# Kernel optimization log

Hardware: AMD Instinct MI355X
Metric: run time of the kernel (lower is better)

Reference implementation:

```python
import jax, jax.numpy as jnp
import numpy as np

HEADS = 8
DIM_HEAD = 64
EPS = 1e-5

def setup_inputs() -> dict:
    key = jax.random.key(0)
    ks = jax.random.split(key, 5)
    c, inner = 320, HEADS * DIM_HEAD
    s = 0.02
    return {
        "hidden_states": jax.random.normal(ks[0], (4, c, 16, 32, 32), jnp.float32),
        "ln_w": jnp.ones((c,), jnp.float32),
        "ln_b": jnp.zeros((c,), jnp.float32),
        "Wq": jax.random.normal(ks[1], (inner, c), jnp.float32) * s,
        "Wk": jax.random.normal(ks[2], (inner, c), jnp.float32) * s,
        "Wv": jax.random.normal(ks[3], (inner, c), jnp.float32) * s,
        "Wo": jax.random.normal(ks[4], (c, inner), jnp.float32) * s,
        "bo": jnp.zeros((c,), jnp.float32),
    }

def reference(hidden_states, ln_w, ln_b, Wq, Wk, Wv, Wo, bo):
    b, c, t, h, w = hidden_states.shape
    scale = DIM_HEAD ** (-0.5)
    # (b h w) t c
    x0 = jnp.transpose(hidden_states, (0, 3, 4, 2, 1)).reshape(b * h * w, t, c)
    # LayerNorm over channel dim
    mu = jnp.mean(x0, axis=-1, keepdims=True)
    var = jnp.var(x0, axis=-1, keepdims=True)
    xn = (x0 - mu) / jnp.sqrt(var + EPS) * ln_w + ln_b
    # QKV projections (self-attention: encoder_hidden_states = normed hidden)
    q = xn @ Wq.T  # [B, t, inner]
    k = xn @ Wk.T
    v = xn @ Wv.T
    B = b * h * w
    q = q.reshape(B, t, HEADS, DIM_HEAD)
    k = k.reshape(B, t, HEADS, DIM_HEAD)
    v = v.reshape(B, t, HEADS, DIM_HEAD)
    scores = jnp.einsum("bqhd,bkhd->bhqk", q, k) * scale
    probs = jax.nn.softmax(scores, axis=-1)
    out = jnp.einsum("bhqk,bkhd->bqhd", probs, v).reshape(B, t, HEADS * DIM_HEAD)
    out = out @ Wo.T + bo
    out = out + x0  # residual (dropout p=0)
    # back to b c t h w
    return jnp.transpose(out.reshape(b, h, w, t, c), (0, 4, 3, 1, 2))
```

## Files before the change

kernel.cpp:

```cpp
#include <hip/hip_runtime.h>

#define TT 16
#define CC 320
#define NHEADS 8
#define DH 64
#define INNER 512

typedef float f32x4 __attribute__((ext_vector_type(4)));
typedef float f32x16 __attribute__((ext_vector_type(16)));
typedef short bf16x8 __attribute__((ext_vector_type(8)));
typedef unsigned short u16;

#define Z16 {0.f,0.f,0.f,0.f,0.f,0.f,0.f,0.f,0.f,0.f,0.f,0.f,0.f,0.f,0.f,0.f}

__device__ __forceinline__ float bf2f(u16 u){
    union { unsigned int i; float f; } v; v.i = ((unsigned int)u) << 16; return v.f;
}
__device__ __forceinline__ u16 f2bf(float f){
    union { float f; unsigned int i; } v; v.f = f;
    unsigned int x = v.i;
    return (u16)((x + 0x7fffu + ((x >> 16) & 1u)) >> 16);
}

__global__ __launch_bounds__(256) void k_wqkv32(const float* __restrict__ wq, const float* __restrict__ wk,
                                                const float* __restrict__ wv, u16* __restrict__ dst){
    int gid  = blockIdx.x * 256 + threadIdx.x;
    int lane = gid & 63;
    int f    = gid >> 6;
    int local = f % 12;
    int kl   = local & 1;
    int nblk = local >> 1;
    int c    = (f / 12) % 10;
    int hd   = f / 120;
    int kk   = c * 2 + kl;
    const float* W = (nblk < 2) ? wq : (nblk < 4) ? wk : wv;
    int n  = hd * DH + (nblk & 1) * 32 + (lane & 31);
    int k0 = kk * 16 + (lane >> 5) * 8;
    const float* src = W + (size_t)n * CC + k0;
    f32x4 v0 = *(const f32x4*)src;
    f32x4 v1 = *(const f32x4*)(src + 4);
    bf16x8 o;
    o[0] = (short)f2bf(v0[0]); o[1] = (short)f2bf(v0[1]);
    o[2] = (short)f2bf(v0[2]); o[3] = (short)f2bf(v0[3]);
    o[4] = (short)f2bf(v1[0]); o[5] = (short)f2bf(v1[1]);
    o[6] = (short)f2bf(v1[2]); o[7] = (short)f2bf(v1[3]);
    *(bf16x8*)(dst + (size_t)gid * 8) = o;
}

__global__ __launch_bounds__(256) void k_wo16(const float* __restrict__ wo, u16* __restrict__ dst){
    int idx  = blockIdx.x * 256 + threadIdx.x;
    int lane = idx & 63;
    int blk  = idx >> 6;
    int KT = INNER / 32;
    int n  = (blk / KT) * 16 + (lane & 15);
    int k0 = (blk % KT) * 32 + (lane >> 4) * 8;
    const float* src = wo + (size_t)n * INNER + k0;
    f32x4 v0 = *(const f32x4*)src;
    f32x4 v1 = *(const f32x4*)(src + 4);
    bf16x8 o;
    o[0] = (short)f2bf(v0[0]); o[1] = (short)f2bf(v0[1]);
    o[2] = (short)f2bf(v0[2]); o[3] = (short)f2bf(v0[3]);
    o[4] = (short)f2bf(v1[0]); o[5] = (short)f2bf(v1[1]);
    o[6] = (short)f2bf(v1[2]); o[7] = (short)f2bf(v1[3]);
    *(bf16x8*)(dst + (size_t)idx * 8) = o;
}

__global__ __launch_bounds__(256) void k_ln(const float* __restrict__ x, const float* __restrict__ lnw,
                                            const float* __restrict__ lnb, u16* __restrict__ xnf){
    __shared__ float tile[CC][37];
    __shared__ float psum[32][36];
    __shared__ float psq[32][36];
    __shared__ float meanb[32];
    __shared__ float rstdb[32];

    int wg = blockIdx.x;
    int t = wg & 15, h = (wg >> 4) & 31, b = wg >> 9;
    int tid = threadIdx.x;
    const size_t base = ((size_t)(b * CC) * TT + t) * 1024 + h * 32;

    int w4 = (tid & 7) * 4, cg = tid >> 3;
    f32x4 s4 = {0.f,0.f,0.f,0.f}, q4 = {0.f,0.f,0.f,0.f};
    for (int i = 0; i < 10; ++i){
        int c = cg * 10 + i;
        f32x4 v = *(const f32x4*)(x + base + (size_t)c * 16384 + w4);
        tile[c][w4 + 0] = v[0]; tile[c][w4 + 1] = v[1];
        tile[c][w4 + 2] = v[2]; tile[c][w4 + 3] = v[3];
        s4 += v; q4 += v * v;
    }
    psum[cg][w4 + 0] = s4[0]; psum[cg][w4 + 1] = s4[1]; psum[cg][w4 + 2] = s4[2]; psum[cg][w4 + 3] = s4[3];
    psq [cg][w4 + 0] = q4[0]; psq [cg][w4 + 1] = q4[1]; psq [cg][w4 + 2] = q4[2]; psq [cg][w4 + 3] = q4[3];
    __syncthreads();

    if (tid < 32){
        float s = 0.f, q = 0.f;
        for (int g = 0; g < 32; ++g){ s += psum[g][tid]; q += psq[g][tid]; }
        float mean = s * (1.f / CC);
        float var  = q * (1.f / CC) - mean * mean;
        meanb[tid] = mean;
        rstdb[tid] = rsqrtf(var + 1e-5f);
    }
    __syncthreads();

    int cl = tid & 63, wq_ = tid >> 6;
    float lw[5], lb[5];
    #pragma unroll
    for (int ci = 0; ci < 5; ++ci){ lw[ci] = lnw[ci * 64 + cl]; lb[ci] = lnb[ci * 64 + cl]; }
    int s_base = (b * 32 + h) * 32;
    for (int wi = 0; wi < 8; ++wi){
        int w = wq_ * 8 + wi;
        float mean = meanb[w], rstd = rstdb[w];
        int s = s_base + w;
        int row = ((s & 1) << 4) | t;
        size_t m32 = (size_t)(s >> 1);
        #pragma unroll
        for (int ci = 0; ci < 5; ++ci){
            int c = ci * 64 + cl;
            float nv = (tile[c][w] - mean) * rstd * lw[ci] + lb[ci];
            int lane = ((((c & 15) >> 3)) << 5) | row;
            xnf[((m32 * 20 + (c >> 4)) * 64 + lane) * 8 + (c & 7)] = f2bf(nv);
        }
    }
}

#define QH(w,s,r,c) smem[((((w)*2+(s))*16+(r))*72) + (c)]
#define KH(w,s,r,c) smem[9216 + ((((w)*2+(s))*16+(r))*72) + (c)]
#define VT(w,s,d,k) smem[18432 + ((((w)*2+(s))*64+(d))*36) + (k)]

__global__ __attribute__((amdgpu_flat_work_group_size(256, 256), amdgpu_waves_per_eu(2, 2)))
void k_attn(const u16* __restrict__ xnf,
            const u16* __restrict__ wqkv,
            u16* __restrict__ aof){
    __shared__ u16 smem[36864];

    const int tid  = threadIdx.x;
    const int lane = tid & 63;
    const int wid  = tid >> 6;
    const int l31  = lane & 31;
    const int h32  = lane >> 5;
    const int l15  = lane & 15;
    const int g4   = lane >> 4;
    const int m32  = blockIdx.x * 4 + wid;
    const f32x4 zero4 = {0.f, 0.f, 0.f, 0.f};

    #pragma unroll
    for (int j = 0; j < 32; ++j){
        int idx = j * 64 + lane;
        int smp = idx >> 10;
        int d   = (idx >> 4) & 63;
        VT(wid, smp, d, 16 + (idx & 15)) = 0;
    }

    bf16x8 a_f[20];
    {
        const u16* xp = xnf + ((size_t)m32 * 20 * 64 + lane) * 8;
        #pragma unroll
        for (int kk = 0; kk < 20; ++kk)
            a_f[kk] = *(const bf16x8*)(xp + kk * 512);
    }

    #define STAGE(hd_, c_) do {                                                        \
        const u16* gsrc_ = wqkv + ((size_t)((hd_) * 10 + (c_)) * 6144);                \
        u16* ldst_ = (u16*)smem + ((c_) & 1) * 6144;                                   \
        _Pragma("unroll")                                                              \
        for (int i_ = 0; i_ < 3; ++i_)                                                 \
            __builtin_amdgcn_global_load_lds(                                          \
                (const __attribute__((address_space(1))) void*)(gsrc_ + (tid + i_ * 256) * 8), \
                (__attribute__((address_space(3))) void*)(ldst_ + (tid + i_ * 256) * 8),       \
                16, 0, 0);                                                             \
    } while (0)

    for (int hd = 0; hd < NHEADS; ++hd){
        __builtin_amdgcn_sched_barrier(0);
        __builtin_amdgcn_s_barrier();
        __builtin_amdgcn_sched_barrier(0);

        STAGE(hd, 0);

        f32x16 acc[6];
        #pragma unroll
        for (int nb = 0; nb < 6; ++nb) acc[nb] = (f32x16)Z16;

        #pragma unroll
        for (int c = 0; c < 10; ++c){
            asm volatile("s_waitcnt vmcnt(0)" ::: "memory");
            __builtin_amdgcn_sched_barrier(0);
            __builtin_amdgcn_s_barrier();
            __builtin_amdgcn_sched_barrier(0);
            if (c < 9) STAGE(hd, c + 1);
            const u16* wb = (const u16*)smem + (c & 1) * 6144;
            #pragma unroll
            for (int kl = 0; kl < 2; ++kl){
                #pragma unroll
                for (int nb = 0; nb < 6; ++nb){
                    bf16x8 b = *(const bf16x8*)(wb + (nb * 2 + kl) * 512 + lane * 8);
                    acc[nb] = __builtin_amdgcn_mfma_f32_32x32x16_bf16(a_f[c * 2 + kl], b, acc[nb], 0, 0, 0);
                }
            }
            __builtin_amdgcn_sched_barrier(0);
            __builtin_amdgcn_s_barrier();
            __builtin_amdgcn_sched_barrier(0);
        }

        #pragma unroll
        for (int r = 0; r < 16; ++r){
            int row = (r & 3) + 8 * (r >> 2) + 4 * h32;
            int smp = row >> 4, tr = row & 15;
            QH(wid, smp, tr, l31)      = f2bf(acc[0][r] * 0.125f);
            QH(wid, smp, tr, 32 + l31) = f2bf(acc[1][r] * 0.125f);
            KH(wid, smp, tr, l31)      = f2bf(acc[2][r]);
            KH(wid, smp, tr, 32 + l31) = f2bf(acc[3][r]);
            VT(wid, smp, l31, tr)      = f2bf(acc[4][r]);
            VT(wid, smp, 32 + l31, tr) = f2bf(acc[5][r]);
        }

        #pragma unroll
        for (int smp = 0; smp < 2; ++smp){
            f32x4 sc = zero4;
            #pragma unroll
            for (int k0 = 0; k0 < DH; k0 += 32){
                bf16x8 qa = *(const bf16x8*)&QH(wid, smp, l15, k0 + g4 * 8);
                bf16x8 kb = *(const bf16x8*)&KH(wid, smp, l15, k0 + g4 * 8);
                sc = __builtin_amdgcn_mfma_f32_16x16x32_bf16(qa, kb, sc, 0, 0, 0);
            }
            f32x4 pr;
            #pragma unroll
            for (int r = 0; r < 4; ++r){
                float m = sc[r];
                m = fmaxf(m, __shfl_xor(m, 1)); m = fmaxf(m, __shfl_xor(m, 2));
                m = fmaxf(m, __shfl_xor(m, 4)); m = fmaxf(m, __shfl_xor(m, 8));
                float e = __expf(sc[r] - m);
                float ss = e;
                ss += __shfl_xor(ss, 1); ss += __shfl_xor(ss, 2);
                ss += __shfl_xor(ss, 4); ss += __shfl_xor(ss, 8);
                pr[r] = e / ss;
            }
            #pragma unroll
            for (int r = 0; r < 4; ++r){
                QH(wid, smp, g4 * 4 + r, l15) = f2bf(pr[r]);
                QH(wid, smp, g4 * 4 + r, 16 + l15) = 0;
            }
            bf16x8 pa = *(const bf16x8*)&QH(wid, smp, l15, g4 * 8);
            #pragma unroll
            for (int nb = 0; nb < 4; ++nb){
                bf16x8 vb = *(const bf16x8*)&VT(wid, smp, nb * 16 + l15, g4 * 8);
                f32x4 at = __builtin_amdgcn_mfma_f32_16x16x32_bf16(pa, vb, zero4, 0, 0, 0);
                #pragma unroll
                for (int r = 0; r < 4; ++r)
                    KH(wid, smp, g4 * 4 + r, nb * 16 + l15) = f2bf(at[r]);
            }
            const size_t sg = (size_t)m32 * 2 + smp;
            #pragma unroll
            for (int kkl = 0; kkl < 2; ++kkl){
                bf16x8 o8 = *(const bf16x8*)&KH(wid, smp, l15, kkl * 32 + g4 * 8);
                *(bf16x8*)(aof + ((sg * 16 + hd * 2 + kkl) * 64 + lane) * 8) = o8;
            }
        }
    }
    #undef STAGE
}

__global__ __launch_bounds__(512, 4) void k_oproj(const u16* __restrict__ aof, const u16* __restrict__ wof,
                                                  const float* __restrict__ bo, u16* __restrict__ proj){
    const int tid  = threadIdx.x;
    const int lane = tid & 63;
    const int wid  = tid >> 6;
    const int l15  = lane & 15;
    const int g4   = lane >> 4;
    const int mh   = wid >> 1;
    const int nh   = wid & 1;
    const size_t mt0 = (size_t)blockIdx.x * 8 + mh * 2;
    const size_t m0  = mt0 * 16;

    f32x4 acc[10][2];
    #pragma unroll
    for (int j = 0; j < 10; ++j){
        acc[j][0] = (f32x4){0.f,0.f,0.f,0.f};
        acc[j][1] = (f32x4){0.f,0.f,0.f,0.f};
    }

    const u16* ap = aof + (mt0 * 16 * 64 + lane) * 8;
    const u16* wp = wof + (((size_t)nh * 10 * 16) * 64 + lane) * 8;

    #pragma unroll 2
    for (int kk = 0; kk < 16; ++kk){
        bf16x8 a0 = *(const bf16x8*)(ap + kk * 512);
        bf16x8 a1 = *(const bf16x8*)(ap + (16 + kk) * 512);
        #pragma unroll
        for (int j = 0; j < 10; ++j){
            bf16x8 b = *(const bf16x8*)(wp + (j * 16 + kk) * 512);
            acc[j][0] = __builtin_amdgcn_mfma_f32_16x16x32_bf16(a0, b, acc[j][0], 0, 0, 0);
            acc[j][1] = __builtin_amdgcn_mfma_f32_16x16x32_bf16(a1, b, acc[j][1], 0, 0, 0);
        }
    }

    #pragma unroll
    for (int j = 0; j < 10; ++j){
        int c = nh * 160 + j * 16 + l15;
        float bias = bo[c];
        #pragma unroll
        for (int mb = 0; mb < 2; ++mb){
            size_t row0 = m0 + mb * 16 + g4 * 4;
            #pragma unroll
            for (int r = 0; r < 4; ++r)
                proj[(row0 + r) * CC + c] = f2bf(acc[j][mb][r] + bias);
        }
    }
}

__global__ __launch_bounds__(256) void k_res(const u16* __restrict__ proj, const float* __restrict__ x,
                                             float* __restrict__ out){
    __shared__ u16 tile[32][328];
    int wg = blockIdx.x;
    int t = wg & 15, h = (wg >> 4) & 31, b = wg >> 9;
    int tid = threadIdx.x;
    int s0 = (b * 32 + h) * 32;
    #pragma unroll
    for (int i = 0; i < 5; ++i){
        int ch = tid + 256 * i;
        int w = ch / 40, cc8 = (ch % 40) * 8;
        *(bf16x8*)(&tile[w][cc8]) = *(const bf16x8*)(proj + ((size_t)(s0 + w) * TT + t) * CC + cc8);
    }
    __syncthreads();
    int w = tid & 31, cq = tid >> 5;
    size_t base = ((size_t)(b * CC) * TT + t) * 1024 + h * 32 + w;
    for (int i = 0; i < 40; ++i){
        int c = cq * 40 + i;
        size_t idx = base + (size_t)c * 16384;
        out[idx] = x[idx] + bf2f(tile[w][c]);
    }
}

extern "C" void kernel_launch(void* const* d_in, const int* in_sizes, int n_in,
                              void* d_out, int out_size, void* d_ws, size_t ws_size,
                              hipStream_t stream){
    const float* hid = (const float*)d_in[0];
    const float* lnw = (const float*)d_in[1];
    const float* lnb = (const float*)d_in[2];
    const float* Wq  = (const float*)d_in[3];
    const float* Wk  = (const float*)d_in[4];
    const float* Wv  = (const float*)d_in[5];
    const float* Wo  = (const float*)d_in[6];
    const float* bo  = (const float*)d_in[7];

    char* ws = (char*)d_ws;
    u16* wqkv = (u16*)ws;
    u16* wo_f = wqkv + (size_t)960 * 512;
    u16* ao   = wo_f + 163840;
    u16* xn   = ao + (size_t)65536 * INNER;
    u16* proj = xn;

    k_wqkv32<<<240, 256, 0, stream>>>(Wq, Wk, Wv, wqkv);
    k_wo16  <<<80, 256, 0, stream>>>(Wo, wo_f);
    k_ln    <<<2048, 256, 0, stream>>>(hid, lnw, lnb, xn);
    k_attn  <<<512, 256, 0, stream>>>(xn, wqkv, ao);
    k_oproj <<<512, 512, 0, stream>>>(ao, wo_f, bo, proj);
    k_res   <<<2048, 256, 0, stream>>>(proj, hid, (float*)d_out);
}
```

Measured before the change: 229.4 us.

## Fuse output projection into attention kernel, dropping attention-output round trip

The per-head attention output is no longer written to global memory and re-read by a separate output-projection kernel. Each wave now accumulates the Wo projection directly with 32x32x16 MFMAs into 10 register accumulators across all heads, then writes biased bf16 results. The Wo weight repack is changed to the 32-row MFMA fragment layout. This removes a 64 MB bf16 intermediate and one launch, but adds 160 accumulator registers to a kernel that already holds 20 A fragments under a 2-waves-per-EU limit, which risks spills or lower overlap. Wo fragments are also read from global inside the head loop.

```diff
diff --git a/kernel.cpp b/kernel.cpp
--- a/kernel.cpp
+++ b/kernel.cpp
@@ -47,13 +47,14 @@
     *(bf16x8*)(dst + (size_t)gid * 8) = o;
 }
 
-__global__ __launch_bounds__(256) void k_wo16(const float* __restrict__ wo, u16* __restrict__ dst){
-    int idx  = blockIdx.x * 256 + threadIdx.x;
-    int lane = idx & 63;
-    int blk  = idx >> 6;
-    int KT = INNER / 32;
-    int n  = (blk / KT) * 16 + (lane & 15);
-    int k0 = (blk % KT) * 32 + (lane >> 4) * 8;
+__global__ __launch_bounds__(256) void k_wo32(const float* __restrict__ wo, u16* __restrict__ dst){
+    int gid  = blockIdx.x * 256 + threadIdx.x;
+    int lane = gid & 63;
+    int f    = gid >> 6;
+    int kt   = f & 31;
+    int nb   = f >> 5;
+    int n  = nb * 32 + (lane & 31);
+    int k0 = kt * 16 + (lane >> 5) * 8;
     const float* src = wo + (size_t)n * INNER + k0;
     f32x4 v0 = *(const f32x4*)src;
     f32x4 v1 = *(const f32x4*)(src + 4);
@@ -62,7 +63,7 @@
     o[2] = (short)f2bf(v0[2]); o[3] = (short)f2bf(v0[3]);
     o[4] = (short)f2bf(v1[0]); o[5] = (short)f2bf(v1[1]);
     o[6] = (short)f2bf(v1[2]); o[7] = (short)f2bf(v1[3]);
-    *(bf16x8*)(dst + (size_t)idx * 8) = o;
+    *(bf16x8*)(dst + (size_t)gid * 8) = o;
 }
 
 __global__ __launch_bounds__(256) void k_ln(const float* __restrict__ x, const float* __restrict__ lnw,
@@ -129,7 +130,9 @@
 __global__ __attribute__((amdgpu_flat_work_group_size(256, 256), amdgpu_waves_per_eu(2, 2)))
 void k_attn(const u16* __restrict__ xnf,
             const u16* __restrict__ wqkv,
-            u16* __restrict__ aof){
+            const u16* __restrict__ wof,
+            const float* __restrict__ bo,
+            u16* __restrict__ proj){
     __shared__ u16 smem[36864];
 
     const int tid  = threadIdx.x;
@@ -157,6 +160,14 @@
         for (int kk = 0; kk < 20; ++kk)
             a_f[kk] = *(const bf16x8*)(xp + kk * 512);
     }
+
+    float bias[10];
+    #pragma unroll
+    for (int nb = 0; nb < 10; ++nb) bias[nb] = bo[nb * 32 + l31];
+
+    f32x16 acco[10];
+    #pragma unroll
+    for (int nb = 0; nb < 10; ++nb) acco[nb] = (f32x16)Z16;
 
     #define STAGE(hd_, c_) do {                                                        \
         const u16* gsrc_ = wqkv + ((size_t)((hd_) * 10 + (c_)) * 6144);                \
@@ -248,61 +259,33 @@
                 for (int r = 0; r < 4; ++r)
                     KH(wid, smp, g4 * 4 + r, nb * 16 + l15) = f2bf(at[r]);
             }
-            const size_t sg = (size_t)m32 * 2 + smp;
-            #pragma unroll
-            for (int kkl = 0; kkl < 2; ++kkl){
-                bf16x8 o8 = *(const bf16x8*)&KH(wid, smp, l15, kkl * 32 + g4 * 8);
-                *(bf16x8*)(aof + ((sg * 16 + hd * 2 + kkl) * 64 + lane) * 8) = o8;
+        }
+
+        {
+            bf16x8 af[4];
+            #pragma unroll
+            for (int kt = 0; kt < 4; ++kt)
+                af[kt] = *(const bf16x8*)&KH(wid, l31 >> 4, l31 & 15, kt * 16 + h32 * 8);
+            #pragma unroll
+            for (int nb = 0; nb < 10; ++nb){
+                #pragma unroll
+                for (int kt = 0; kt < 4; ++kt){
+                    bf16x8 b = *(const bf16x8*)(wof + ((size_t)(nb * 32 + hd * 4 + kt) * 64 + lane) * 8);
+                    acco[nb] = __builtin_amdgcn_mfma_f32_32x32x16_bf16(af[kt], b, acco[nb], 0, 0, 0);
+                }
             }
         }
     }
     #undef STAGE
-}
-
-__global__ __launch_bounds__(512, 4) void k_oproj(const u16* __restrict__ aof, const u16* __restrict__ wof,
-                                                  const float* __restrict__ bo, u16* __restrict__ proj){
-    const int tid  = threadIdx.x;
-    const int lane = tid & 63;
-    const int wid  = tid >> 6;
-    const int l15  = lane & 15;
-    const int g4   = lane >> 4;
-    const int mh   = wid >> 1;
-    const int nh   = wid & 1;
-    const size_t mt0 = (size_t)blockIdx.x * 8 + mh * 2;
-    const size_t m0  = mt0 * 16;
-
-    f32x4 acc[10][2];
-    #pragma unroll
-    for (int j = 0; j < 10; ++j){
-        acc[j][0] = (f32x4){0.f,0.f,0.f,0.f};
-        acc[j][1] = (f32x4){0.f,0.f,0.f,0.f};
-    }
-
-    const u16* ap = aof + (mt0 * 16 * 64 + lane) * 8;
-    const u16* wp = wof + (((size_t)nh * 10 * 16) * 64 + lane) * 8;
-
-    #pragma unroll 2
-    for (int kk = 0; kk < 16; ++kk){
-        bf16x8 a0 = *(const bf16x8*)(ap + kk * 512);
-        bf16x8 a1 = *(const bf16x8*)(ap + (16 + kk) * 512);
-        #pragma unroll
-        for (int j = 0; j < 10; ++j){
-            bf16x8 b = *(const bf16x8*)(wp + (j * 16 + kk) * 512);
-            acc[j][0] = __builtin_amdgcn_mfma_f32_16x16x32_bf16(a0, b, acc[j][0], 0, 0, 0);
-            acc[j][1] = __builtin_amdgcn_mfma_f32_16x16x32_bf16(a1, b, acc[j][1], 0, 0, 0);
-        }
-    }
-
-    #pragma unroll
-    for (int j = 0; j < 10; ++j){
-        int c = nh * 160 + j * 16 + l15;
-        float bias = bo[c];
-        #pragma unroll
-        for (int mb = 0; mb < 2; ++mb){
-            size_t row0 = m0 + mb * 16 + g4 * 4;
-            #pragma unroll
-            for (int r = 0; r < 4; ++r)
-                proj[(row0 + r) * CC + c] = f2bf(acc[j][mb][r] + bias);
+
+    const size_t rbase = (size_t)m32 * 32;
+    #pragma unroll
+    for (int nb = 0; nb < 10; ++nb){
+        float bn = bias[nb];
+        #pragma unroll
+        for (int r = 0; r < 16; ++r){
+            int row = (r & 3) + 8 * (r >> 2) + 4 * h32;
+            proj[(rbase + row) * CC + nb * 32 + l31] = f2bf(acco[nb][r] + bn);
         }
     }
 }
@@ -345,14 +328,12 @@
     char* ws = (char*)d_ws;
     u16* wqkv = (u16*)ws;
     u16* wo_f = wqkv + (size_t)960 * 512;
-    u16* ao   = wo_f + 163840;
-    u16* xn   = ao + (size_t)65536 * INNER;
-    u16* proj = xn;
+    u16* xn   = wo_f + 163840;
+    u16* proj = xn + (size_t)65536 * CC;
 
     k_wqkv32<<<240, 256, 0, stream>>>(Wq, Wk, Wv, wqkv);
-    k_wo16  <<<80, 256, 0, stream>>>(Wo, wo_f);
+    k_wo32  <<<80, 256, 0, stream>>>(Wo, wo_f);
     k_ln    <<<2048, 256, 0, stream>>>(hid, lnw, lnb, xn);
-    k_attn  <<<512, 256, 0, stream>>>(xn, wqkv, ao);
-    k_oproj <<<512, 512, 0, stream>>>(ao, wo_f, bo, proj);
+    k_attn  <<<512, 256, 0, stream>>>(xn, wqkv, wo_f, bo, proj);
     k_res   <<<2048, 256, 0, stream>>>(proj, hid, (float*)d_out);
 }
```

After: 390.3 us. 70.2% more time.
